# Optimization experiments

Hardware: AMD Instinct MI355X
Metric: run time of the kernel (lower is better)

## Reference

```python
import jax, jax.numpy as jnp
import numpy as np
from jax import lax

EPS = 1e-12
N_ITER = 25
PAD = 1
GROUPS = 4


def conv2d(x, w, padding, groups):
    # x: NCHW, w: OIHW (I = C // groups)
    return lax.conv_general_dilated(
        x, w, (1, 1), ((padding, padding), (padding, padding)),
        dimension_numbers=('NCHW', 'OIHW', 'NCHW'), feature_group_count=groups)


def conv_transpose2d(h, w, padding, groups):
    # stride-1 transposed conv == conv with spatially flipped, in/out-swapped kernel
    O, Ig, kh, kw = w.shape
    I = Ig * groups
    wt = w.reshape(groups, O // groups, Ig, kh, kw).transpose(0, 2, 1, 3, 4)
    wt = wt.reshape(I, O // groups, kh, kw)[:, :, ::-1, ::-1]
    return conv2d(h, wt, kh - 1 - padding, groups)


def nnmf_conv2d(x, weight, n_iterations=N_ITER, padding=PAD, groups=GROUPS,
                normalize_channels=True):
    # non-negative, L1-normalized (per output channel) weights
    w = jnp.abs(weight)
    w = w / (w.sum(axis=(1, 2, 3), keepdims=True) + EPS)
    # non-negative input, normalized over channels
    x = x / (x.sum(axis=1, keepdims=True) + EPS)
    N, C, H, W = x.shape
    O = weight.shape[0]
    h0 = jnp.full((N, O, H, W), 1.0 / O, dtype=x.dtype)

    def body(i, h):
        recon = conv_transpose2d(h, w, padding, groups)   # back-projection
        ratio = x / (recon + EPS)
        h = h * conv2d(ratio, w, padding, groups)         # multiplicative update
        if normalize_channels:
            h = h / (h.sum(axis=1, keepdims=True) + EPS)
        return h

    return lax.fori_loop(0, n_iterations, body, h0)


def layernorm_cf(x, w, b, eps=1e-6):
    # channels_first LayerNorm over C of NCHW
    u = x.mean(axis=1, keepdims=True)
    s = jnp.mean((x - u) ** 2, axis=1, keepdims=True)
    xn = (x - u) * lax.rsqrt(s + eps)
    return w[None, :, None, None] * xn + b[None, :, None, None]


def layernorm_last(x, w, b, eps=1e-5):
    u = x.mean(axis=-1, keepdims=True)
    s = jnp.mean((x - u) ** 2, axis=-1, keepdims=True)
    return (x - u) * lax.rsqrt(s + eps) * w + b


def setup_inputs() -> dict:
    key = jax.random.key(0)
    ks = jax.random.split(key, 8)
    C, Hd = 96, 384  # dim, mlp hidden = 4*embed_dim
    x = jax.random.normal(ks[0], (8, C, 56, 56), dtype=jnp.float32)
    return {
        'x': x,
        'ln1_w': jnp.ones((C,), jnp.float32),
        'ln1_b': jnp.zeros((C,), jnp.float32),
        'w_nnmf': jax.random.uniform(ks[1], (C, C // GROUPS, 3, 3), jnp.float32, 0.01, 1.0),
        'ln2_w': jnp.ones((C,), jnp.float32),
        'ln2_b': jnp.zeros((C,), jnp.float32),
        'w1': jax.random.normal(ks[2], (C, Hd), jnp.float32) * 0.02,
        'b1': jnp.zeros((Hd,), jnp.float32),
        'w2': jax.random.normal(ks[3], (Hd, C), jnp.float32) * 0.02,
        'b2': jnp.zeros((C,), jnp.float32),
    }


def reference(x, ln1_w, ln1_b, w_nnmf, ln2_w, ln2_b, w1, b1, w2, b2):
    # attn branch (NNMF conv on relu'd channels-first layernorm)
    x_norm = layernorm_cf(x, ln1_w, ln1_b)
    x = x + nnmf_conv2d(jax.nn.relu(x_norm), w_nnmf)
    # MLP branch, channels-last
    xl = jnp.transpose(x, (0, 2, 3, 1))  # NHWC
    h = layernorm_last(xl, ln2_w, ln2_b)
    h = jax.nn.gelu(h @ w1 + b1, approximate=False) @ w2 + b2
    xl = xl + h
    return jnp.transpose(xl, (0, 3, 1, 2))
```

## Files before the change

### kernel.cpp

```cpp
#include <hip/hip_runtime.h>
#include <math.h>
#include <string.h>

typedef unsigned short ushort_t;
typedef __attribute__((ext_vector_type(8))) short bhalf8;
typedef __attribute__((ext_vector_type(4))) float floatx4;

#define NN    8
#define CC_   96
#define HH    56
#define WW    56
#define HWHW  (HH*WW)
#define NPIX  (NN*HWHW)
#define NELEM (NN*CC_*HWHW)
#define GROUPS 4
#define IG    24
#define NITER 25
#define EPSV  1e-12f
#define TS    40

__device__ __forceinline__ unsigned bf2pack(float a, float b) {
    unsigned ua = __float_as_uint(a), ub = __float_as_uint(b);
    ua += 0x7fffu + ((ua >> 16) & 1u);
    ub += 0x7fffu + ((ub >> 16) & 1u);
    return (ua >> 16) | (ub & 0xffff0000u);
}
__device__ __forceinline__ ushort_t bf1pack(float a) {
    unsigned ua = __float_as_uint(a);
    ua += 0x7fffu + ((ua >> 16) & 1u);
    return (ushort_t)(ua >> 16);
}
__device__ __forceinline__ float bflo(unsigned u) { return __uint_as_float(u << 16); }
__device__ __forceinline__ float bfhi(unsigned u) { return __uint_as_float(u & 0xffff0000u); }

__device__ __forceinline__ float rcpf(float x) {
    float r;
    asm("v_rcp_f32 %0, %1" : "=v"(r) : "v"(x));
    return r;
}

__device__ __forceinline__ int swz(int slot, int u) {
    return slot*TS + u;
}

__global__ __launch_bounds__(256) void prep_kernel(
        const float* __restrict__ w_in,
        ushort_t* __restrict__ WfP, ushort_t* __restrict__ WtP,
        const float* __restrict__ w1, const float* __restrict__ w2,
        ushort_t* __restrict__ w1P, ushort_t* __restrict__ w2P,
        const float* __restrict__ x, const float* __restrict__ lw1,
        const float* __restrict__ lb1, unsigned* __restrict__ Xp) {
    __shared__ float wn[24*216];
    __shared__ float rsum[24];
    int b = blockIdx.x;
    int tid = threadIdx.x;

    if (b < 4) {
        int g = b;
        if (tid < 24) {
            const float* wr = w_in + (size_t)(g*24 + tid)*216;
            float s = 0.f;
            for (int j = 0; j < 216; ++j) s += fabsf(wr[j]);
            rsum[tid] = s;
        }
        __syncthreads();
        for (int i = tid; i < 24*216; i += 256) {
            int row = i / 216;
            wn[i] = fabsf(w_in[(size_t)g*24*216 + i]) * rcpf(rsum[row] + EPSV);
        }
        __syncthreads();
        int lg = tid >> 6;
        int lane = tid & 63;
        int quad = lane >> 4, nn15 = lane & 15;
        #pragma unroll 1
        for (int i = 0; i < 9; ++i) {
            int fr  = lg + 4*i;
            int sel = fr / 18;
            int rem = fr % 18;
            int ot  = rem & 1;
            int tap = rem >> 1;
            int m = ot*16 + nn15;
            ushort_t v[8];
            #pragma unroll
            for (int j = 0; j < 8; ++j) {
                int kc = quad*8 + j;
                float val = 0.f;
                if (m < IG && kc < IG) {
                    if (sel == 0) val = wn[m*216 + kc*9 + tap];
                    else          val = wn[kc*216 + m*9 + (8 - tap)];
                }
                v[j] = bf1pack(val);
            }
            ushort_t* dst = (sel ? WtP : WfP) + ((size_t)((g*9 + tap)*2 + ot)*64 + lane)*8;
            *(uint4*)dst = *(uint4*)v;
        }
    } else if (b < 40) {
        int f = (b - 4)*4 + (tid >> 6);
        int lane = tid & 63;
        int quad = lane >> 4, nn15 = lane & 15;
        ushort_t v[8];
        if (f < 72) {
            int nt = f / 3, ks = f % 3;
            #pragma unroll
            for (int j = 0; j < 8; ++j)
                v[j] = bf1pack(w1[(size_t)(ks*32 + quad*8 + j)*384 + nt*16 + nn15]);
            *(uint4*)(w1P + ((size_t)f*64 + lane)*8) = *(uint4*)v;
        } else {
            int f2 = f - 72;
            int mt = f2 / 12, ks = f2 % 12;
            #pragma unroll
            for (int j = 0; j < 8; ++j)
                v[j] = bf1pack(w2[(size_t)(ks*32 + quad*8 + j)*96 + mt*16 + nn15]);
            *(uint4*)(w2P + ((size_t)f2*64 + lane)*8) = *(uint4*)v;
        }
    } else {
        int p = (b - 40)*256 + tid;
        int n = p / HWHW, hw = p % HWHW;
        const float* xp = x + (size_t)n*CC_*HWHW + hw;
        float s = 0.f, ss = 0.f;
        for (int c = 0; c < CC_; ++c) { float v = xp[(size_t)c*HWHW]; s += v; ss += v*v; }
        float u  = s * (1.f/CC_);
        float var = ss * (1.f/CC_) - u*u;
        float rs = rsqrtf(var + 1e-6f);
        float sr = 0.f;
        for (int c = 0; c < CC_; ++c) {
            float v = xp[(size_t)c*HWHW];
            float a = fmaxf((v-u)*rs*lw1[c] + lb1[c], 0.f);
            sr += a;
        }
        float inv = 1.f / (sr + EPSV);
        for (int c = 0; c < CC_; c += 4) {
            float a[4];
            #pragma unroll
            for (int j = 0; j < 4; ++j) {
                float v = xp[(size_t)(c+j)*HWHW];
                a[j] = fmaxf((v-u)*rs*lw1[c+j] + lb1[c+j], 0.f) * inv;
            }
            int g = c / IG, pr2 = (c % IG) >> 2;
            uint2 pk; pk.x = bf2pack(a[0], a[1]); pk.y = bf2pack(a[2], a[3]);
            *(uint2*)&Xp[2*(((size_t)(n*4+g)*6 + pr2)*HWHW + hw)] = pk;
        }
    }
}

__global__ __launch_bounds__(512, 4) void nnmf_mfma_kernel(
        const unsigned* __restrict__ HupI, unsigned* __restrict__ HupO,
        const float* __restrict__ Scur, float* __restrict__ Snxt,
        const ushort_t* __restrict__ WtP, const ushort_t* __restrict__ WfP,
        const unsigned* __restrict__ Xp,
        int it0, unsigned huInit, float sInit) {
    __shared__ ushort_t hn[352*TS];
    __shared__ ushort_t rt_[288*TS];
    __shared__ float sacc[392];
    int b    = blockIdx.x;
    int k_   = b >> 3;
    int ng   = (b & 7)*4 + (k_ >> 4);
    int tile = k_ & 15;
    int rtb  = tile >> 1;
    int half = tile & 1;
    int n    = ng >> 2;
    int g    = ng & 3;
    int tid  = threadIdx.x;
    int r0   = rtb*7;
    int xb   = half*28;
    unsigned plane6 = (unsigned)(n*4 + g)*6;

    int waveId = tid >> 6, lane = tid & 63;
    int quad = lane >> 4, nn = lane & 15;
    int otB = waveId & 1;
    int mbB = otB*16 + quad*4;

    bhalf8 afrB[9];
    {
        const ushort_t* ap = WtP + ((size_t)(g*9*2 + otB)*64 + lane)*8;
        #pragma unroll
        for (int t = 0; t < 9; ++t) afrB[t] = *(const bhalf8*)(ap + (size_t)t*2*64*8);
    }

    uint2 raw[6];
    float sSum[6];
    #pragma unroll
    for (int kk = 0; kk < 6; ++kk) {
        int idx = tid + kk*512;
        uint2 rv = {0u, 0u};
        float st = 0.f;
        if (idx < 2816) {
            int pr2  = idx / 352;
            int slot = idx - pr2*352;
            int r = slot >> 5, q = slot & 31;
            int gr = r0 - 2 + r, gc = xb - 2 + q;
            if (!it0 && pr2 < 6 && gr >= 0 && gr < HH && gc >= 0 && gc < WW) {
                unsigned off = (unsigned)(gr*WW + gc);
                unsigned pix = (unsigned)(n*HWHW) + off;
                rv = *(const uint2*)&HupI[2*((size_t)(plane6 + pr2)*HWHW + off)];
                float4 sv = *(const float4*)&Scur[4*(size_t)pix];
                st = sv.x + sv.y + sv.z + sv.w;
            }
        }
        raw[kk] = rv;
        sSum[kk] = st;
    }

    #pragma unroll
    for (int kk = 0; kk < 6; ++kk) {
        int idx = tid + kk*512;
        if (idx < 2816) {
            int pr2  = idx / 352;
            int slot = idx - pr2*352;
            int r = slot >> 5, q = slot & 31;
            int gr = r0 - 2 + r, gc = xb - 2 + q;
            uint2 pk = {0u, 0u};
            if (pr2 < 6 && gr >= 0 && gr < HH && gc >= 0 && gc < WW) {
                if (it0) {
                    float si = rcpf(4.f*sInit + EPSV);
                    float hval = bflo(huInit) * si;
                    pk.x = bf2pack(hval, hval);
                    pk.y = pk.x;
                } else {
                    float si = rcpf(sSum[kk] + EPSV);
                    pk.x = bf2pack(bflo(raw[kk].x)*si, bfhi(raw[kk].x)*si);
                    pk.y = bf2pack(bflo(raw[kk].y)*si, bfhi(raw[kk].y)*si);
                }
            }
            *(uint2*)&hn[swz(slot, 4*pr2)] = pk;
        }
    }
    if (tid < 288) *(uint4*)&rt_[swz(tid, 24)] = (uint4){0u,0u,0u,0u};
    __syncthreads();

    {
        #pragma unroll
        for (int i = 0; i < 5; ++i) {
            int tk = waveId + 8*i;
            if (tk < 36) {
                int pt  = (tk >> 1) & 1;
                int row = tk >> 2;
                int x0R = pt*14;
                unsigned xa = 0u, xc = 0u;
                int gr = r0 - 1 + row, gc = xb - 1 + x0R + nn;
                if (mbB < IG && gr >= 0 && gr < HH && gc >= 0 && gc < WW) {
                    unsigned off = (unsigned)(gr*WW + gc);
                    uint2 xv = *(const uint2*)&Xp[2*((size_t)(plane6 + (mbB >> 2))*HWHW + off)];
                    xa = xv.x; xc = xv.y;
                }
                floatx4 acc = (floatx4){0.f,0.f,0.f,0.f};
                #pragma unroll
                for (int t = 0; t < 9; ++t) {
                    int ky = t / 3, kx = t % 3;
                    bhalf8 bfr = *(const bhalf8*)
                        &hn[swz((row + ky)*32 + kx + nn + x0R, quad*8)];
                    acc = __builtin_amdgcn_mfma_f32_16x16x32_bf16(afrB[t], bfr, acc, 0, 0, 0);
                }
                if (mbB < IG) {
                    int slot = row*32 + x0R + nn;
                    *(unsigned*)&rt_[swz(slot, mbB)] =
                        bf2pack(bflo(xa)*rcpf(acc[0]+EPSV), bfhi(xa)*rcpf(acc[1]+EPSV));
                    *(unsigned*)&rt_[swz(slot, mbB + 2)] =
                        bf2pack(bflo(xc)*rcpf(acc[2]+EPSV), bfhi(xc)*rcpf(acc[3]+EPSV));
                }
            }
        }
    }
    __syncthreads();

    {
        const ushort_t* ap = WfP + ((size_t)(g*9*2 + otB)*64 + lane)*8;
        bhalf8 afr[9];
        #pragma unroll
        for (int t = 0; t < 9; ++t) afr[t] = *(const bhalf8*)(ap + (size_t)t*2*64*8);
        int mb = mbB;

        #pragma unroll
        for (int i = 0; i < 4; ++i) {
            int tc = waveId + 8*i;
            if (tc < 28) {
                int xt = (tc >> 1) & 1;
                int w  = tc >> 2;
                int px0 = xt*12;
                floatx4 acc = (floatx4){0.f,0.f,0.f,0.f};
                #pragma unroll
                for (int t = 0; t < 9; ++t) {
                    int ky = t / 3, kx = t % 3;
                    bhalf8 bfr = *(const bhalf8*)
                        &rt_[swz((w + ky)*32 + kx + nn + px0, quad*8)];
                    acc = __builtin_amdgcn_mfma_f32_16x16x32_bf16(afr[t], bfr, acc, 0, 0, 0);
                }

                int grow = r0 + w;
                int pxh = px0 + nn;
                float psum = 0.f;
                if (mb < IG) {
                    unsigned off = (unsigned)(grow*WW + xb + pxh);
                    uint2 hv = *(const uint2*)&hn[swz((w + 2)*32 + pxh + 2, mb)];
                    float h0 = bflo(hv.x) * acc[0];
                    float h1 = bfhi(hv.x) * acc[1];
                    float h2 = bflo(hv.y) * acc[2];
                    float h3 = bfhi(hv.y) * acc[3];
                    uint2 po; po.x = bf2pack(h0, h1); po.y = bf2pack(h2, h3);
                    *(uint2*)&HupO[2*((size_t)(plane6 + (mb >> 2))*HWHW + off)] = po;
                    psum = h0 + h1 + h2 + h3;
                }
                psum += __shfl_down(psum, 32, 64);
                psum += __shfl_down(psum, 16, 64);
                if (lane < 16) sacc[otB*196 + w*28 + pxh] = psum;
            }
        }
    }
    __syncthreads();
    if (tid < 196) {
        unsigned pix = (unsigned)(n*HWHW + (r0 + tid/28)*WW + xb + (tid % 28));
        Snxt[4*(size_t)pix + g] = sacc[tid] + sacc[196 + tid];
    }
}

__global__ __launch_bounds__(256) void mlpres_kernel(
        const float* __restrict__ x, const unsigned* __restrict__ Hup,
        const float* __restrict__ S4,
        const float* __restrict__ lw, const float* __restrict__ lb,
        const ushort_t* __restrict__ w1P, const float* __restrict__ b1,
        const ushort_t* __restrict__ w2P, const float* __restrict__ b2,
        float* __restrict__ out) {
    __shared__ ushort_t lh[32*392];
    __shared__ unsigned xln[32*52];
    __shared__ float vt[96*34];
    __shared__ float redS[8*32], redSS[8*32];
    __shared__ float uArr[32], rsArr[32];
    int blk = blockIdx.x;
    int tid = threadIdx.x;
    int p0  = blk * 32;
    int n   = p0 / HWHW;
    int hw0 = p0 % HWHW;

    {
        int px = tid & 31, cg = tid >> 5;
        int p  = p0 + px, hw = hw0 + px;
        float4 sv = *(const float4*)&S4[4*(size_t)p];
        float stot = sv.x + sv.y + sv.z + sv.w;
        float sinv = 1.f / (stot + EPSV);
        int g = cg >> 1;
        unsigned plane6 = (unsigned)(n*4 + g)*6 + (unsigned)((cg & 1)*3);
        size_t xbase = (size_t)n*CC_*HWHW + hw;
        float v[12];
        float s = 0.f, ss = 0.f;
        #pragma unroll
        for (int j2 = 0; j2 < 3; ++j2) {
            int c = cg*12 + 4*j2;
            uint2 hu = *(const uint2*)&Hup[2*((size_t)(plane6 + j2)*HWHW + hw)];
            float h[4] = { bflo(hu.x), bfhi(hu.x), bflo(hu.y), bfhi(hu.y) };
            #pragma unroll
            for (int j = 0; j < 4; ++j) {
                float vv = x[xbase + (size_t)(c+j)*HWHW] + h[j] * sinv;
                v[4*j2 + j] = vv;
                s += vv; ss += vv*vv;
            }
        }
        redS[cg*32 + px] = s; redSS[cg*32 + px] = ss;
        __syncthreads();
        if (tid < 32) {
            float S_ = 0.f, SS_ = 0.f;
            #pragma unroll
            for (int k = 0; k < 8; ++k) { S_ += redS[k*32 + tid]; SS_ += redSS[k*32 + tid]; }
            float u  = S_ * (1.f/CC_);
            float var = SS_ * (1.f/CC_) - u*u;
            uArr[tid] = u; rsArr[tid] = rsqrtf(var + 1e-5f);
        }
        __syncthreads();
        float u = uArr[px], rs = rsArr[px];
        #pragma unroll
        for (int j = 0; j < 6; ++j) {
            int c = cg*12 + 2*j;
            float a0 = (v[2*j]   - u)*rs*lw[c]   + lb[c];
            float a1 = (v[2*j+1] - u)*rs*lw[c+1] + lb[c+1];
            xln[px*52 + cg*6 + j] = bf2pack(a0, a1);
            vt[c*34 + px]     = v[2*j];
            vt[(c+1)*34 + px] = v[2*j+1];
        }
    }
    __syncthreads();

    int wv  = tid >> 6, lane = tid & 63;
    int quad = lane >> 4, nn = lane & 15;
    int tt  = wv >> 1;
    int hv_ = wv & 1;

    bhalf8 a1[3];
    #pragma unroll
    for (int ks = 0; ks < 3; ++ks)
        a1[ks] = *(const bhalf8*)&xln[(tt*16 + nn)*52 + ks*16 + quad*4];

    #pragma unroll 1
    for (int i = 0; i < 12; ++i) {
        int nt = hv_*12 + i;
        floatx4 acc = (floatx4){0.f,0.f,0.f,0.f};
        #pragma unroll
        for (int ks = 0; ks < 3; ++ks) {
            bhalf8 bfr = *(const bhalf8*)(w1P + ((size_t)(nt*3 + ks)*64 + lane)*8);
            acc = __builtin_amdgcn_mfma_f32_16x16x32_bf16(a1[ks], bfr, acc, 0, 0, 0);
        }
        float b1v = b1[nt*16 + nn];
        #pragma unroll
        for (int r = 0; r < 4; ++r) {
            float h = acc[r] + b1v;
            h = 0.5f * h * (1.f + erff(h * 0.70710678118654752440f));
            lh[(tt*16 + quad*4 + r)*392 + nt*16 + nn] = bf1pack(h);
        }
    }
    __syncthreads();

    bhalf8 bf2[12];
    #pragma unroll
    for (int ks = 0; ks < 12; ++ks)
        bf2[ks] = *(const bhalf8*)&lh[(tt*16 + nn)*392 + ks*32 + quad*8];

    #pragma unroll 1
    for (int i = 0; i < 3; ++i) {
        int mt = hv_*3 + i;
        floatx4 acc = (floatx4){0.f,0.f,0.f,0.f};
        #pragma unroll
        for (int ks = 0; ks < 12; ++ks) {
            bhalf8 af = *(const bhalf8*)(w2P + ((size_t)(mt*12 + ks)*64 + lane)*8);
            acc = __builtin_amdgcn_mfma_f32_16x16x32_bf16(af, bf2[ks], acc, 0, 0, 0);
        }
        #pragma unroll
        for (int r = 0; r < 4; ++r) {
            int c = mt*16 + quad*4 + r;
            size_t addr = ((size_t)n*CC_ + c)*HWHW + hw0 + tt*16 + nn;
            out[addr] = vt[c*34 + tt*16 + nn] + (acc[r] + b2[c]);
        }
    }
}

extern "C" void kernel_launch(void* const* d_in, const int* in_sizes, int n_in,
                              void* d_out, int out_size, void* d_ws, size_t ws_size,
                              hipStream_t stream) {
    const float* x    = (const float*)d_in[0];
    const float* ln1w = (const float*)d_in[1];
    const float* ln1b = (const float*)d_in[2];
    const float* wnn  = (const float*)d_in[3];
    const float* ln2w = (const float*)d_in[4];
    const float* ln2b = (const float*)d_in[5];
    const float* w1   = (const float*)d_in[6];
    const float* b1   = (const float*)d_in[7];
    const float* w2   = (const float*)d_in[8];
    const float* b2   = (const float*)d_in[9];
    float* out = (float*)d_out;
    char* ws = (char*)d_ws;

    ushort_t* WfP  = (ushort_t*)ws;                   ws += 73728*2;
    ushort_t* WtP  = (ushort_t*)ws;                   ws += 73728*2;
    ushort_t* w1P  = (ushort_t*)ws;                   ws += 36864*2;
    ushort_t* w2P  = (ushort_t*)ws;                   ws += 36864*2;
    unsigned* Xp   = (unsigned*)ws;                   ws += (size_t)(NELEM/2)*4;
    unsigned* Hu0  = (unsigned*)ws;                   ws += (size_t)(NELEM/2)*4;
    unsigned* Hu1  = (unsigned*)ws;                   ws += (size_t)(NELEM/2)*4;
    float*    SA   = (float*)ws;                      ws += (size_t)4*NPIX*4;
    float*    SB   = (float*)ws;                      ws += (size_t)4*NPIX*4;

    union { float f; unsigned u; } cv; cv.f = 1.f/96.f;
    unsigned ur = cv.u + 0x7fffu + ((cv.u >> 16) & 1u);
    unsigned short hbits = (unsigned short)(ur >> 16);
    unsigned huInit = ((unsigned)hbits << 16) | hbits;
    union { float f; unsigned u; } hv; hv.u = ((unsigned)hbits) << 16;
    float sInit = 24.f * hv.f;

    prep_kernel<<<138, 256, 0, stream>>>(wnn, WfP, WtP, w1, w2, w1P, w2P,
                                         x, ln1w, ln1b, Xp);

    for (int it = 0; it < NITER; ++it) {
        const unsigned* HuI  = (it & 1) ? Hu1 : Hu0;
        unsigned*       HuO  = (it & 1) ? Hu0 : Hu1;
        const float*    Scur = (it & 1) ? SB : SA;
        float*          Snxt = (it & 1) ? SA : SB;
        nnmf_mfma_kernel<<<512, 512, 0, stream>>>(HuI, HuO, Scur, Snxt, WtP, WfP, Xp,
                                                  (it == 0) ? 1 : 0, huInit, sInit);
    }

    mlpres_kernel<<<NPIX/32, 256, 0, stream>>>(x, Hu1, SB, ln2w, ln2b,
                                               w1P, b1, w2P, b2, out);
}
```

Before: 392.4 us.

## Write per-wave partial channel sums directly, split MFMA accumulators into even/odd chains

The shared-memory channel-sum staging buffer and its final block barrier are removed. Each wave now writes its partial sum straight to a sum buffer that is twice as wide (8 floats per pixel), and readers add the 8 partials. The 9-tap MFMA chains are split into two independent accumulators to shorten the dependency chain, and the ratio store becomes one 64-bit LDS write. The cost is twice the sum-buffer traffic and scattered 4-byte global stores.

Measured after the change: 401.1 us. 2.2% more time.

```diff
diff --git a/kernel.cpp b/kernel.cpp
--- a/kernel.cpp
+++ b/kernel.cpp
@@ -151,7 +151,6 @@
         int it0, unsigned huInit, float sInit) {
     __shared__ ushort_t hn[352*TS];
     __shared__ ushort_t rt_[288*TS];
-    __shared__ float sacc[392];
     int b    = blockIdx.x;
     int k_   = b >> 3;
     int ng   = (b & 7)*4 + (k_ >> 4);
@@ -193,8 +192,11 @@
                 unsigned off = (unsigned)(gr*WW + gc);
                 unsigned pix = (unsigned)(n*HWHW) + off;
                 rv = *(const uint2*)&HupI[2*((size_t)(plane6 + pr2)*HWHW + off)];
-                float4 sv = *(const float4*)&Scur[4*(size_t)pix];
-                st = sv.x + sv.y + sv.z + sv.w;
+                float4 sa = *(const float4*)&Scur[8*(size_t)pix];
+                float4 sb = *(const float4*)&Scur[8*(size_t)pix + 4];
+                float g0 = sa.x + sa.y, g1 = sa.z + sa.w;
+                float g2 = sb.x + sb.y, g3 = sb.z + sb.w;
+                st = ((g0 + g1) + g2) + g3;
             }
         }
         raw[kk] = rv;
@@ -243,20 +245,25 @@
                     uint2 xv = *(const uint2*)&Xp[2*((size_t)(plane6 + (mbB >> 2))*HWHW + off)];
                     xa = xv.x; xc = xv.y;
                 }
-                floatx4 acc = (floatx4){0.f,0.f,0.f,0.f};
+                floatx4 ace = (floatx4){0.f,0.f,0.f,0.f};
+                floatx4 aco = (floatx4){0.f,0.f,0.f,0.f};
                 #pragma unroll
                 for (int t = 0; t < 9; ++t) {
                     int ky = t / 3, kx = t % 3;
                     bhalf8 bfr = *(const bhalf8*)
                         &hn[swz((row + ky)*32 + kx + nn + x0R, quad*8)];
-                    acc = __builtin_amdgcn_mfma_f32_16x16x32_bf16(afrB[t], bfr, acc, 0, 0, 0);
-                }
+                    if (t & 1)
+                        aco = __builtin_amdgcn_mfma_f32_16x16x32_bf16(afrB[t], bfr, aco, 0, 0, 0);
+                    else
+                        ace = __builtin_amdgcn_mfma_f32_16x16x32_bf16(afrB[t], bfr, ace, 0, 0, 0);
+                }
+                floatx4 acc = ace + aco;
                 if (mbB < IG) {
                     int slot = row*32 + x0R + nn;
-                    *(unsigned*)&rt_[swz(slot, mbB)] =
-                        bf2pack(bflo(xa)*rcpf(acc[0]+EPSV), bfhi(xa)*rcpf(acc[1]+EPSV));
-                    *(unsigned*)&rt_[swz(slot, mbB + 2)] =
-                        bf2pack(bflo(xc)*rcpf(acc[2]+EPSV), bfhi(xc)*rcpf(acc[3]+EPSV));
+                    uint2 ro;
+                    ro.x = bf2pack(bflo(xa)*rcpf(acc[0]+EPSV), bfhi(xa)*rcpf(acc[1]+EPSV));
+                    ro.y = bf2pack(bflo(xc)*rcpf(acc[2]+EPSV), bfhi(xc)*rcpf(acc[3]+EPSV));
+                    *(uint2*)&rt_[swz(slot, mbB)] = ro;
                 }
             }
         }
@@ -277,14 +284,19 @@
                 int xt = (tc >> 1) & 1;
                 int w  = tc >> 2;
                 int px0 = xt*12;
-                floatx4 acc = (floatx4){0.f,0.f,0.f,0.f};
+                floatx4 ace = (floatx4){0.f,0.f,0.f,0.f};
+                floatx4 aco = (floatx4){0.f,0.f,0.f,0.f};
                 #pragma unroll
                 for (int t = 0; t < 9; ++t) {
                     int ky = t / 3, kx = t % 3;
                     bhalf8 bfr = *(const bhalf8*)
                         &rt_[swz((w + ky)*32 + kx + nn + px0, quad*8)];
-                    acc = __builtin_amdgcn_mfma_f32_16x16x32_bf16(afr[t], bfr, acc, 0, 0, 0);
-                }
+                    if (t & 1)
+                        aco = __builtin_amdgcn_mfma_f32_16x16x32_bf16(afr[t], bfr, aco, 0, 0, 0);
+                    else
+                        ace = __builtin_amdgcn_mfma_f32_16x16x32_bf16(afr[t], bfr, ace, 0, 0, 0);
+                }
+                floatx4 acc = ace + aco;
 
                 int grow = r0 + w;
                 int pxh = px0 + nn;
@@ -302,20 +314,18 @@
                 }
                 psum += __shfl_down(psum, 32, 64);
                 psum += __shfl_down(psum, 16, 64);
-                if (lane < 16) sacc[otB*196 + w*28 + pxh] = psum;
-            }
-        }
-    }
-    __syncthreads();
-    if (tid < 196) {
-        unsigned pix = (unsigned)(n*HWHW + (r0 + tid/28)*WW + xb + (tid % 28));
-        Snxt[4*(size_t)pix + g] = sacc[tid] + sacc[196 + tid];
+                if (lane < 16) {
+                    unsigned pix = (unsigned)(n*HWHW + grow*WW + xb + pxh);
+                    Snxt[8*(size_t)pix + 2*g + otB] = psum;
+                }
+            }
+        }
     }
 }
 
 __global__ __launch_bounds__(256) void mlpres_kernel(
         const float* __restrict__ x, const unsigned* __restrict__ Hup,
-        const float* __restrict__ S4,
+        const float* __restrict__ S8,
         const float* __restrict__ lw, const float* __restrict__ lb,
         const ushort_t* __restrict__ w1P, const float* __restrict__ b1,
         const ushort_t* __restrict__ w2P, const float* __restrict__ b2,
@@ -334,8 +344,11 @@
     {
         int px = tid & 31, cg = tid >> 5;
         int p  = p0 + px, hw = hw0 + px;
-        float4 sv = *(const float4*)&S4[4*(size_t)p];
-        float stot = sv.x + sv.y + sv.z + sv.w;
+        float4 sa = *(const float4*)&S8[8*(size_t)p];
+        float4 sb = *(const float4*)&S8[8*(size_t)p + 4];
+        float g0 = sa.x + sa.y, g1 = sa.z + sa.w;
+        float g2 = sb.x + sb.y, g3 = sb.z + sb.w;
+        float stot = ((g0 + g1) + g2) + g3;
         float sinv = 1.f / (stot + EPSV);
         int g = cg >> 1;
         unsigned plane6 = (unsigned)(n*4 + g)*6 + (unsigned)((cg & 1)*3);
@@ -453,8 +466,8 @@
     unsigned* Xp   = (unsigned*)ws;                   ws += (size_t)(NELEM/2)*4;
     unsigned* Hu0  = (unsigned*)ws;                   ws += (size_t)(NELEM/2)*4;
     unsigned* Hu1  = (unsigned*)ws;                   ws += (size_t)(NELEM/2)*4;
-    float*    SA   = (float*)ws;                      ws += (size_t)4*NPIX*4;
-    float*    SB   = (float*)ws;                      ws += (size_t)4*NPIX*4;
+    float*    SA   = (float*)ws;                      ws += (size_t)8*NPIX*4;
+    float*    SB   = (float*)ws;                      ws += (size_t)8*NPIX*4;
 
     union { float f; unsigned u; } cv; cv.f = 1.f/96.f;
     unsigned ur = cv.u + 0x7fffu + ((cv.u >> 16) & 1u);
```
